# Kernel optimization log

Measured on AMD Instinct MI355X. Metric: run time of the kernel, lower is better.

Reference implementation:

```python
import jax, jax.numpy as jnp
import numpy as np

B, T, EMB, NDIM = 8, 2048, 1024, 1024


def setup_inputs() -> dict:
    key = jax.random.key(0)
    k1, k2, k3, k4 = jax.random.split(key, 4)
    X = jax.random.normal(k1, (B, T, EMB), dtype=jnp.float32)
    # Linear(emb, ndim, bias=False); stored as [emb, ndim] so projection is X @ W.
    scale = 1.0 / np.sqrt(EMB)
    Wq = jax.random.normal(k2, (EMB, NDIM), dtype=jnp.float32) * scale
    Wk = jax.random.normal(k3, (EMB, NDIM), dtype=jnp.float32) * scale
    Wv = jax.random.normal(k4, (EMB, NDIM), dtype=jnp.float32) * scale
    return {"X": X, "Wq": Wq, "Wk": Wk, "Wv": Wv}


def reference(X, Wq, Wk, Wv):
    ndim = Wq.shape[-1]
    T_ = X.shape[1]
    Q = X @ Wq  # [B,T,ndim]
    K = X @ Wk  # [B,T,ndim]
    V = X @ Wv  # [B,T,ndim]
    # scores[b,t,s] = Q[b,t] . K[b,s], scaled by ndim^-0.5
    scores = jnp.einsum("btd,bsd->bts", Q, K) * (ndim ** -0.5)
    mask = jnp.tril(jnp.ones((T_, T_), dtype=bool))  # causal lower-triangular
    scores = jnp.where(mask, scores, -jnp.inf)
    # NOTE: source uses F.softmax(..., dim=1) -> normalize over the QUERY axis
    # (columns of the [T,T] matrix), not the usual key axis. Replicated faithfully.
    probs = jax.nn.softmax(scores, axis=1)
    # dropout is identity in eval / p=0 deterministic baseline
    return probs @ V  # [B,T,ndim]
```

## Files before the change

kernel.cpp:

```cpp
#include <hip/hip_runtime.h>
#include <hip/hip_bf16.h>

#define B_   8
#define T_   2048
#define EMB_ 1024
#define ND_  1024
#define NTB2 8

typedef __attribute__((ext_vector_type(8))) short   bf8_t;
typedef __attribute__((ext_vector_type(4))) float   f32x4;

__device__ __forceinline__ unsigned short f2bf(float f) {
  union { float f; unsigned int u; } c; c.f = f;
  unsigned int u = c.u;
  unsigned int r = (u + 0x7FFFu + ((u >> 16) & 1u)) >> 16;
  return (unsigned short)r;
}

__device__ __forceinline__ float bf2f(unsigned short b) {
  union { unsigned int u; float f; } c; c.u = ((unsigned int)b) << 16;
  return c.f;
}

__device__ __forceinline__ void gload_lds16(const unsigned short* g, unsigned short* l) {
  __builtin_amdgcn_global_load_lds(
      (const __attribute__((address_space(1))) unsigned int*)g,
      (__attribute__((address_space(3))) unsigned int*)l,
      16, 0, 0);
}

#define SB0() __builtin_amdgcn_sched_barrier(0)
#define BAR() __builtin_amdgcn_s_barrier()

__device__ __forceinline__ void stage_half(const unsigned short* __restrict__ g, int lda,
                                           unsigned short* lhalf, int wave, int lane) {
  const int r3 = lane >> 3, c3 = lane & 7;
  const int colsw = ((c3 ^ r3) << 3);
#pragma unroll
  for (int j = 0; j < 2; ++j) {
    const int row = wave * 8 + r3 + 64 * j;
    gload_lds16(g + (size_t)row * lda + colsw, lhalf + wave * 512 + j * 4096);
  }
}

__device__ __forceinline__ bf8_t read_frag(const unsigned short* half, int r, int ks, int lane) {
  const int col = (((ks) << 5) + ((lane >> 4) << 3)) ^ ((r & 7) << 3);
  return *(const bf8_t*)(half + r * 64 + col);
}

__device__ __forceinline__ int swz_ep(int x) { return ((x >> 1) & 7) << 4; }

__global__ void __launch_bounds__(256) cvt_x_kernel(const float* __restrict__ in,
                                                    unsigned short* __restrict__ out) {
  const int i = (blockIdx.x * 256 + threadIdx.x) * 4;
  float4 v = *(const float4*)(in + i);
  ushort4 o = make_ushort4(f2bf(v.x), f2bf(v.y), f2bf(v.z), f2bf(v.w));
  *(ushort4*)(out + i) = o;
}

__global__ void __launch_bounds__(256) transpose_w3_kernel(const float* __restrict__ Wq,
                                                           const float* __restrict__ Wk,
                                                           const float* __restrict__ Wv,
                                                           unsigned short* __restrict__ Wt3) {
  __shared__ unsigned short tile[32][33];
  const int z = blockIdx.z;
  const float* W = (z == 0) ? Wq : (z == 1) ? Wk : Wv;
  const float cscale = (z == 0) ? 0.03125f : 1.0f;
  unsigned short* Wt = Wt3 + (size_t)z * ND_ * EMB_;
  const int n0 = blockIdx.x * 32, k0 = blockIdx.y * 32;
  const int tx = threadIdx.x & 31, ty = threadIdx.x >> 5;
#pragma unroll
  for (int r = 0; r < 32; r += 8) {
    float v = W[(size_t)(k0 + ty + r) * ND_ + n0 + tx];
    tile[tx][ty + r] = f2bf(v * cscale);
  }
  __syncthreads();
#pragma unroll
  for (int r = 0; r < 32; r += 8) {
    Wt[(size_t)(n0 + ty + r) * EMB_ + k0 + tx] = tile[ty + r][tx];
  }
}

#define MFMA_QUAD(MB, AF, AOFF) do { \
  __builtin_amdgcn_s_setprio(1); \
  _Pragma("unroll") \
  for (int mi = 0; mi < 2; ++mi) \
    _Pragma("unroll") \
    for (int nf = 0; nf < 4; ++nf) \
      _Pragma("unroll") \
      for (int ks = 0; ks < 2; ++ks) \
        acc[(MB) * 2 + mi][nf] = __builtin_amdgcn_mfma_f32_16x16x32_bf16( \
            (AF)[(AOFF) + mi][ks], bfr[nf][ks], acc[(MB) * 2 + mi][nf], 0, 0, 0); \
  __builtin_amdgcn_s_setprio(0); \
} while (0)

#define MFMA_Q8(MB) do { \
  __builtin_amdgcn_s_setprio(1); \
  _Pragma("unroll") \
  for (int nf = 0; nf < 4; ++nf) \
    _Pragma("unroll") \
    for (int ks = 0; ks < 2; ++ks) \
      acc[(MB)][nf] = __builtin_amdgcn_mfma_f32_16x16x32_bf16( \
          af[(MB)][ks], bfr[nf][ks], acc[(MB)][nf], 0, 0, 0); \
  __builtin_amdgcn_s_setprio(0); \
} while (0)

#define LDSA(d, h) (lds256 + ((d) * 2 + (h)) * 8192)
#define LDSB(d, h) (lds256 + 32768 + ((d) * 2 + (h)) * 8192)

#define GEMM256_LOOP(ABASE, BBASE, LDK) \
  stage_half((ABASE),                             (LDK), LDSA(0, 0), wave, lane); \
  stage_half((ABASE) + (size_t)128 * (LDK),       (LDK), LDSA(0, 1), wave, lane); \
  stage_half((BBASE),                             (LDK), LDSB(0, 0), wave, lane); \
  stage_half((BBASE) + (size_t)128 * (LDK),       (LDK), LDSB(0, 1), wave, lane); \
  stage_half((BBASE) + 64,                        (LDK), LDSB(1, 0), wave, lane); \
  stage_half((BBASE) + (size_t)128 * (LDK) + 64,  (LDK), LDSB(1, 1), wave, lane); \
  stage_half((ABASE) + 64,                        (LDK), LDSA(1, 0), wave, lane); \
  stage_half((ABASE) + (size_t)128 * (LDK) + 64,  (LDK), LDSA(1, 1), wave, lane); \
  asm volatile("s_waitcnt vmcnt(8)" ::: "memory"); \
  SB0(); BAR(); SB0(); \
  for (int t = 0; t < 16; ++t) { \
    const int d = t & 1; \
    const unsigned short* Ah = LDSA(d, wm); \
    const unsigned short* Bh = LDSB(d, wn >> 1); \
    bf8_t bfr[4][2], af[4][2]; \
    _Pragma("unroll") \
    for (int nf = 0; nf < 4; ++nf) \
      _Pragma("unroll") \
      for (int ks = 0; ks < 2; ++ks) bfr[nf][ks] = read_frag(Bh, brow + nf * 16, ks, lane); \
    _Pragma("unroll") \
    for (int mf = 0; mf < 4; ++mf) \
      _Pragma("unroll") \
      for (int ks = 0; ks < 2; ++ks) af[mf][ks] = read_frag(Ah, arow + mf * 16, ks, lane); \
    SB0(); BAR(); SB0(); \
    MFMA_QUAD(0, af, 0); \
    SB0(); \
    asm volatile("s_waitcnt lgkmcnt(0)" ::: "memory"); \
    SB0(); BAR(); SB0(); \
    if (t < 14) { \
      stage_half((BBASE) + (size_t)(t + 2) * 64,                     (LDK), LDSB(d, 0), wave, lane); \
      stage_half((BBASE) + (size_t)128 * (LDK) + (size_t)(t + 2) * 64,(LDK), LDSB(d, 1), wave, lane); \
    } \
    SB0(); BAR(); SB0(); \
    MFMA_QUAD(1, af, 2); \
    SB0(); BAR(); SB0(); \
    bf8_t af2[4][2]; \
    _Pragma("unroll") \
    for (int mf = 0; mf < 4; ++mf) \
      _Pragma("unroll") \
      for (int ks = 0; ks < 2; ++ks) af2[mf][ks] = read_frag(Ah, arow + (mf + 4) * 16, ks, lane); \
    SB0(); BAR(); SB0(); \
    MFMA_QUAD(2, af2, 0); \
    SB0(); \
    asm volatile("s_waitcnt lgkmcnt(0)" ::: "memory"); \
    SB0(); BAR(); SB0(); \
    if (t < 14) { \
      stage_half((ABASE) + (size_t)(t + 2) * 64,                     (LDK), LDSA(d, 0), wave, lane); \
      stage_half((ABASE) + (size_t)128 * (LDK) + (size_t)(t + 2) * 64,(LDK), LDSA(d, 1), wave, lane); \
      asm volatile("s_waitcnt vmcnt(8)" ::: "memory"); \
    } else if (t == 14) { \
      asm volatile("s_waitcnt vmcnt(0)" ::: "memory"); \
    } \
    SB0(); BAR(); SB0(); \
    MFMA_QUAD(3, af2, 2); \
    SB0(); BAR(); SB0(); \
  }

template <int OUTMODE>
__global__ void __launch_bounds__(512, 2)
gemm_xw256_kernel(const unsigned short* __restrict__ A,
                  const unsigned short* __restrict__ Bt,
                  unsigned short* __restrict__ C) {
  extern __shared__ unsigned short lds256[];
  const int tid = threadIdx.x, lane = tid & 63, wave = tid >> 6;
  const int wm = wave >> 2, wn = wave & 3;
  const int m0 = blockIdx.y * 256, n0 = blockIdx.x * 256;
  const unsigned short* Ab = A + (size_t)m0 * EMB_;
  const unsigned short* Bb = Bt + (size_t)n0 * EMB_;
  f32x4 acc[8][4];
#pragma unroll
  for (int i = 0; i < 8; ++i)
#pragma unroll
    for (int j = 0; j < 4; ++j)
#pragma unroll
      for (int q = 0; q < 4; ++q) acc[i][j][q] = 0.f;
  const int arow = lane & 15;
  const int brow = (wn & 1) * 64 + (lane & 15);

  GEMM256_LOOP(Ab, Bb, EMB_)

  const int cc = lane & 15, cr4 = (lane >> 4) << 2;
#pragma unroll
  for (int mf = 0; mf < 8; ++mf)
#pragma unroll
    for (int nf = 0; nf < 4; ++nf)
#pragma unroll
      for (int q = 0; q < 4; ++q) {
        const int r = wm * 128 + mf * 16 + cr4 + q;
        const int c = wn * 64 + nf * 16 + cc;
        const unsigned short bv = f2bf(acc[mf][nf][q]);
        const int byte = (OUTMODE == 1) ? (c * 512 + ((r * 2) ^ swz_ep(c)))
                                        : (r * 512 + ((c * 2) ^ swz_ep(r)));
        lds256[byte >> 1] = bv;
      }
  __syncthreads();
  if (OUTMODE == 0) {
#pragma unroll
    for (int p = 0; p < 16; ++p) {
      const int o = p * 8192 + tid * 16;
      const int ri = o >> 9, cb = o & 511;
      const bf8_t v = *(const bf8_t*)(lds256 + (((o & ~511) | (cb ^ swz_ep(ri))) >> 1));
      *(bf8_t*)(C + (size_t)(m0 + ri) * ND_ + n0 + (cb >> 1)) = v;
    }
  } else {
    const int bb = m0 >> 11, tt0 = m0 & 2047;
#pragma unroll
    for (int p = 0; p < 16; ++p) {
      const int o = p * 8192 + tid * 16;
      const int ci = o >> 9, rb = o & 511;
      const bf8_t v = *(const bf8_t*)(lds256 + (((o & ~511) | (rb ^ swz_ep(ci))) >> 1));
      *(bf8_t*)(C + ((size_t)bb * ND_ + n0 + ci) * T_ + tt0 + (rb >> 1)) = v;
    }
  }
}

__global__ void __launch_bounds__(512, 2)
scoretile576_kernel(const unsigned short* __restrict__ Qb,
                    const unsigned short* __restrict__ Kb,
                    unsigned short* __restrict__ Pp,
                    float* __restrict__ pm) {
  extern __shared__ unsigned short lds256[];
  const int id = blockIdx.x;
  const int b = id & 7;
  const int r = id >> 3;
  int sc = 0, pfx = 0;
#pragma unroll 8
  for (int i = 0; i < 8; ++i) {
    const int cnt = 16 - 2 * sc;
    if (pfx + cnt <= r) { pfx += cnt; ++sc; }
  }
  const int tr = 2 * sc + (r - pfx);
  const int t0 = tr * 128, s0 = sc * 256;
  const int tid = threadIdx.x, lane = tid & 63, wave = tid >> 6;
  const int wm = wave >> 2, wn = wave & 3;
  const int arow = lane & 15;
  const unsigned short* Ab = Qb + ((size_t)b * T_ + t0) * ND_;
  const unsigned short* Bb = Kb + ((size_t)b * T_ + s0) * ND_;
  f32x4 acc[4][4];
#pragma unroll
  for (int i = 0; i < 4; ++i)
#pragma unroll
    for (int j = 0; j < 4; ++j)
#pragma unroll
      for (int q = 0; q < 4; ++q) acc[i][j][q] = 0.f;

  stage_half(Ab,                           ND_, lds256,                     wave, lane);
  stage_half(Bb,                           ND_, lds256 + 16384,             wave, lane);
  stage_half(Bb + (size_t)128 * ND_,       ND_, lds256 + 16384 + 8192,      wave, lane);
  stage_half(Ab + 64,                      ND_, lds256 + 8192,              wave, lane);
  stage_half(Bb + 64,                      ND_, lds256 + 16384 + 2 * 8192,  wave, lane);
  stage_half(Bb + (size_t)128 * ND_ + 64,  ND_, lds256 + 16384 + 3 * 8192,  wave, lane);
  asm volatile("s_waitcnt vmcnt(6)" ::: "memory");
  SB0(); BAR(); SB0();

  for (int t = 0; t < 16; ++t) {
    const int d = t & 1;
    const unsigned short* Ah = lds256 + d * 8192;
    const unsigned short* Bh = lds256 + 16384 + (d * 2 + (wn >> 1)) * 8192;
    bf8_t bfr[4][2], af[4][2];
#pragma unroll
    for (int nf = 0; nf < 4; ++nf)
#pragma unroll
      for (int ks = 0; ks < 2; ++ks)
        bfr[nf][ks] = read_frag(Bh, (wn & 1) * 64 + nf * 16 + arow, ks, lane);
#pragma unroll
    for (int mf = 0; mf < 4; ++mf)
#pragma unroll
      for (int ks = 0; ks < 2; ++ks)
        af[mf][ks] = read_frag(Ah, wm * 64 + mf * 16 + arow, ks, lane);
    SB0(); BAR(); SB0();
    MFMA_Q8(0);
    SB0();
    asm volatile("s_waitcnt lgkmcnt(0)" ::: "memory");
    SB0(); BAR(); SB0();
    if (t < 14) {
      stage_half(Ab + (size_t)(t + 2) * 64, ND_, lds256 + d * 8192, wave, lane);
      stage_half(Bb + (size_t)(t + 2) * 64, ND_, lds256 + 16384 + (d * 2) * 8192, wave, lane);
    }
    SB0(); BAR(); SB0();
    MFMA_Q8(1);
    SB0(); BAR(); SB0();
    if (t < 14)
      stage_half(Bb + (size_t)128 * ND_ + (size_t)(t + 2) * 64, ND_, lds256 + 16384 + (d * 2 + 1) * 8192, wave, lane);
    SB0(); BAR(); SB0();
    MFMA_Q8(2);
    SB0(); BAR(); SB0();
    if (t < 14)      { asm volatile("s_waitcnt vmcnt(6)" ::: "memory"); }
    else if (t == 14){ asm volatile("s_waitcnt vmcnt(0)" ::: "memory"); }
    SB0(); BAR(); SB0();
    MFMA_Q8(3);
    SB0(); BAR(); SB0();
  }

  __syncthreads();
  const int cc = lane & 15, cr4 = (lane >> 4) << 2;
  float csum[4];
#pragma unroll
  for (int nf = 0; nf < 4; ++nf) csum[nf] = 0.f;
#pragma unroll
  for (int mf = 0; mf < 4; ++mf)
#pragma unroll
    for (int nf = 0; nf < 4; ++nf)
#pragma unroll
      for (int q = 0; q < 4; ++q) {
        const int rr = wm * 64 + mf * 16 + cr4 + q;
        const int c  = wn * 64 + nf * 16 + cc;
        const bool ok = (t0 + rr) >= (s0 + c);
        unsigned short bv = 0;
        if (ok) {
          bv = f2bf(__expf(fminf(acc[mf][nf][q], 30.f)));
          csum[nf] += bf2f(bv);
        }
        lds256[(rr * 512 + ((c * 2) ^ swz_ep(rr))) >> 1] = bv;
      }
  __syncthreads();
  unsigned short* Pbase = Pp + (size_t)b * T_ * T_;
#pragma unroll
  for (int p = 0; p < 8; ++p) {
    const int o = p * 8192 + tid * 16;
    const int ri = o >> 9, cb = o & 511;
    const bf8_t v = *(const bf8_t*)(lds256 + (((o & ~511) | (cb ^ swz_ep(ri))) >> 1));
    *(bf8_t*)(Pbase + (size_t)(t0 + ri) * T_ + s0 + (cb >> 1)) = v;
  }
#pragma unroll
  for (int nf = 0; nf < 4; ++nf) {
    csum[nf] += __shfl_xor(csum[nf], 16);
    csum[nf] += __shfl_xor(csum[nf], 32);
  }
  __syncthreads();
  float* red = (float*)lds256;
  if (lane < 16) {
#pragma unroll
    for (int nf = 0; nf < 4; ++nf)
      red[((wm * 4 + wn) * 4 + nf) * 16 + lane] = csum[nf];
  }
  __syncthreads();
  if (wm == 0 && lane < 16) {
    const size_t base = (((size_t)b * 8 + sc) * 16 + tr) * 256;
#pragma unroll
    for (int nf = 0; nf < 4; ++nf) {
      const float s = red[((0 * 4 + wn) * 4 + nf) * 16 + lane] +
                      red[((1 * 4 + wn) * 4 + nf) * 16 + lane];
      pm[base + wn * 64 + nf * 16 + lane] = s;
    }
  }
}

__global__ void __launch_bounds__(256) colreduce_kernel(const float* __restrict__ pm,
                                                        float* __restrict__ colinv) {
  const int sc = blockIdx.x, b = blockIdx.y, c = threadIdx.x;
  float l = 0.f;
  for (int tr = 2 * sc; tr < 16; ++tr)
    l += pm[(((size_t)b * 8 + sc) * 16 + tr) * 256 + c];
  colinv[(size_t)b * T_ + sc * 256 + c] = 1.0f / l;
}

__global__ void __launch_bounds__(256) vscale_kernel(unsigned short* __restrict__ Vt,
                                                     const float* __restrict__ colinv) {
  const int idx = blockIdx.x * 256 + threadIdx.x;
  const int s8 = (idx * 8) & (T_ - 1);
  const int bd = idx / (T_ / 8);
  const int b = bd >> 10;
  unsigned short* p = Vt + (size_t)bd * T_ + s8;
  bf8_t v = *(bf8_t*)p;
#pragma unroll
  for (int j = 0; j < 8; ++j) {
    const float f = bf2f((unsigned short)v[j]) * colinv[(size_t)b * T_ + s8 + j];
    v[j] = (short)f2bf(f);
  }
  *(bf8_t*)p = v;
}

__device__ __forceinline__ void pv_segment(const unsigned short* __restrict__ Ab,
                                           const unsigned short* __restrict__ Bb,
                                           float* __restrict__ Cb,
                                           int ktiles, unsigned short* lds256,
                                           int lane, int wave) {
  const int wm = wave >> 2, wn = wave & 3;
  const int arow = lane & 15;
  f32x4 acc[4][4];
#pragma unroll
  for (int i = 0; i < 4; ++i)
#pragma unroll
    for (int j = 0; j < 4; ++j)
#pragma unroll
      for (int q = 0; q < 4; ++q) acc[i][j][q] = 0.f;

  stage_half(Ab,                           T_, lds256,                     wave, lane);
  stage_half(Bb,                           T_, lds256 + 16384,             wave, lane);
  stage_half(Bb + (size_t)128 * T_,        T_, lds256 + 16384 + 8192,      wave, lane);
  stage_half(Ab + 64,                      T_, lds256 + 8192,              wave, lane);
  stage_half(Bb + 64,                      T_, lds256 + 16384 + 2 * 8192,  wave, lane);
  stage_half(Bb + (size_t)128 * T_ + 64,   T_, lds256 + 16384 + 3 * 8192,  wave, lane);
  asm volatile("s_waitcnt vmcnt(6)" ::: "memory");
  SB0(); BAR(); SB0();

  for (int t = 0; t < ktiles; ++t) {
    const int d = t & 1;
    const unsigned short* Ah = lds256 + d * 8192;
    const unsigned short* Bh = lds256 + 16384 + (d * 2 + (wn >> 1)) * 8192;
    bf8_t bfr[4][2], af[4][2];
#pragma unroll
    for (int nf = 0; nf < 4; ++nf)
#pragma unroll
      for (int ks = 0; ks < 2; ++ks)
        bfr[nf][ks] = read_frag(Bh, (wn & 1) * 64 + nf * 16 + arow, ks, lane);
#pragma unroll
    for (int mf = 0; mf < 4; ++mf)
#pragma unroll
      for (int ks = 0; ks < 2; ++ks)
        af[mf][ks] = read_frag(Ah, wm * 64 + mf * 16 + arow, ks, lane);
    SB0(); BAR(); SB0();
    MFMA_Q8(0);
    SB0();
    asm volatile("s_waitcnt lgkmcnt(0)" ::: "memory");
    SB0(); BAR(); SB0();
    if (t < ktiles - 2) {
      stage_half(Ab + (size_t)(t + 2) * 64, T_, lds256 + d * 8192, wave, lane);
      stage_half(Bb + (size_t)(t + 2) * 64, T_, lds256 + 16384 + (d * 2) * 8192, wave, lane);
    }
    SB0(); BAR(); SB0();
    MFMA_Q8(1);
    SB0(); BAR(); SB0();
    if (t < ktiles - 2)
      stage_half(Bb + (size_t)128 * T_ + (size_t)(t + 2) * 64, T_, lds256 + 16384 + (d * 2 + 1) * 8192, wave, lane);
    SB0(); BAR(); SB0();
    MFMA_Q8(2);
    SB0(); BAR(); SB0();
    if (t < ktiles - 2)      { asm volatile("s_waitcnt vmcnt(6)" ::: "memory"); }
    else if (t == ktiles - 2){ asm volatile("s_waitcnt vmcnt(0)" ::: "memory"); }
    SB0(); BAR(); SB0();
    MFMA_Q8(3);
    SB0(); BAR(); SB0();
  }

  const int cc = lane & 15, cr4 = (lane >> 4) << 2;
#pragma unroll
  for (int mf = 0; mf < 4; ++mf)
#pragma unroll
    for (int nf = 0; nf < 4; ++nf)
#pragma unroll
      for (int q = 0; q < 4; ++q) {
        const int row = wm * 64 + mf * 16 + cr4 + q;
        const int col = wn * 64 + nf * 16 + cc;
        Cb[(size_t)row * ND_ + col] = acc[mf][nf][q];
      }
}

__global__ void __launch_bounds__(512, 2)
gemm_pv256_kernel(const unsigned short* __restrict__ Pb,
                  const unsigned short* __restrict__ Vt,
                  float* __restrict__ out) {
  extern __shared__ unsigned short lds256[];
  const int b = blockIdx.x & 7;
  const int pair = (blockIdx.x >> 3) & 7;
  const int ncol = blockIdx.x >> 6;
  const int lane = threadIdx.x & 63, wave = threadIdx.x >> 6;
  const int tbs[2] = {pair, 15 - pair};
#pragma unroll
  for (int si = 0; si < 2; ++si) {
    const int tb = tbs[si];
    const int ktiles = 2 * tb + 2;
    pv_segment(Pb + (size_t)b * T_ * T_ + (size_t)tb * 128 * T_,
               Vt + (size_t)b * ND_ * T_ + (size_t)ncol * 256 * T_,
               out + (size_t)b * T_ * ND_ + (size_t)tb * 128 * ND_ + ncol * 256,
               ktiles, lds256, lane, wave);
  }
}

extern "C" void kernel_launch(void* const* d_in, const int* in_sizes, int n_in,
                              void* d_out, int out_size, void* d_ws, size_t ws_size,
                              hipStream_t stream) {
  const float* X  = (const float*)d_in[0];
  const float* Wq = (const float*)d_in[1];
  const float* Wk = (const float*)d_in[2];
  const float* Wv = (const float*)d_in[3];
  float* out = (float*)d_out;
  (void)in_sizes; (void)n_in; (void)out_size;

  char* ws = (char*)d_ws;
  size_t off = 0;
  auto alloc = [&](size_t bytes) {
    void* p = ws + off;
    off += (bytes + 255) & ~(size_t)255;
    return p;
  };
  unsigned short* Xb  = (unsigned short*)alloc((size_t)B_ * T_ * EMB_ * 2);
  unsigned short* Wt3 = (unsigned short*)alloc((size_t)3 * ND_ * EMB_ * 2);
  unsigned short* Qb  = (unsigned short*)alloc((size_t)B_ * T_ * ND_ * 2);
  unsigned short* Kb  = (unsigned short*)alloc((size_t)B_ * T_ * ND_ * 2);
  unsigned short* Vt  = (unsigned short*)alloc((size_t)B_ * ND_ * T_ * 2);
  float* colinv = (float*)alloc((size_t)B_ * T_ * 4);
  float* pm     = (float*)alloc((size_t)B_ * 8 * 16 * 256 * 4);
  unsigned short* Pb  = (unsigned short*)alloc((size_t)B_ * T_ * T_ * 2);
  if (off > ws_size) return;

  hipFuncSetAttribute((const void*)&gemm_xw256_kernel<0>,
                      hipFuncAttributeMaxDynamicSharedMemorySize, 131072);
  hipFuncSetAttribute((const void*)&gemm_xw256_kernel<1>,
                      hipFuncAttributeMaxDynamicSharedMemorySize, 131072);
  hipFuncSetAttribute((const void*)&scoretile576_kernel,
                      hipFuncAttributeMaxDynamicSharedMemorySize, 98304);
  hipFuncSetAttribute((const void*)&gemm_pv256_kernel,
                      hipFuncAttributeMaxDynamicSharedMemorySize, 98304);

  hipLaunchKernelGGL(cvt_x_kernel, dim3((B_ * T_ * EMB_) / 1024), dim3(256), 0, stream, X, Xb);
  hipLaunchKernelGGL(transpose_w3_kernel, dim3(32, 32, 3), dim3(256), 0, stream, Wq, Wk, Wv, Wt3);
  hipLaunchKernelGGL((gemm_xw256_kernel<0>), dim3(ND_ / 256, (B_ * T_) / 256), dim3(512), 131072, stream,
                     Xb, Wt3, Qb);
  hipLaunchKernelGGL((gemm_xw256_kernel<0>), dim3(ND_ / 256, (B_ * T_) / 256), dim3(512), 131072, stream,
                     Xb, Wt3 + (size_t)ND_ * EMB_, Kb);
  hipLaunchKernelGGL((gemm_xw256_kernel<1>), dim3(ND_ / 256, (B_ * T_) / 256), dim3(512), 131072, stream,
                     Xb, Wt3 + (size_t)2 * ND_ * EMB_, Vt);
  hipLaunchKernelGGL(scoretile576_kernel, dim3(576), dim3(512), 98304, stream, Qb, Kb, Pb, pm);
  hipLaunchKernelGGL(colreduce_kernel, dim3(8, B_), dim3(256), 0, stream, pm, colinv);
  hipLaunchKernelGGL(vscale_kernel, dim3((B_ * ND_ * T_) / 8 / 256), dim3(256), 0, stream, Vt, colinv);
  hipLaunchKernelGGL(gemm_pv256_kernel, dim3(NTB2 * 4 * B_), dim3(512), 98304, stream, Pb, Vt, out);
}
```

Baseline: 283.0 us.

## Retile causal score kernel to 128x128 triangular tiles with higher occupancy

The score/exp kernel moves from 128x256 tiles (576 blocks) to 128x128 tiles enumerated over the lower triangle with a sqrt-based decode (1088 blocks). Causal masking is applied only on diagonal tiles, and LDS use drops to 64KB so launch bounds allow 4 blocks per CU. The aim is to cut wasted upper-triangle work and improve load balance and occupancy. In exchange, each smaller tile reuses less of what it loads, and the column-sum partials and colreduce are re-laid out for 128-wide column blocks. Blocks just above the diagonal are no longer written as zeros, so correctness depends on the PV GEMM never reading them.

```diff
diff --git a/kernel.cpp b/kernel.cpp
--- a/kernel.cpp
+++ b/kernel.cpp
@@ -29,6 +29,14 @@
       16, 0, 0);
 }
 
+__device__ __forceinline__ void tri_decode(int p, int& tblk, int& sblk) {
+  int t = (int)((sqrtf(8.0f * (float)p + 1.0f) - 1.0f) * 0.5f);
+  while ((t + 1) * (t + 2) / 2 <= p) ++t;
+  while (t * (t + 1) / 2 > p) --t;
+  tblk = t;
+  sblk = p - t * (t + 1) / 2;
+}
+
 #define SB0() __builtin_amdgcn_sched_barrier(0)
 #define BAR() __builtin_amdgcn_s_barrier()
 
@@ -49,6 +57,7 @@
 }
 
 __device__ __forceinline__ int swz_ep(int x) { return ((x >> 1) & 7) << 4; }
+__device__ __forceinline__ int swz_ep2(int r) { return (r & 7) << 4; }
 
 __global__ void __launch_bounds__(256) cvt_x_kernel(const float* __restrict__ in,
                                                     unsigned short* __restrict__ out) {
@@ -98,6 +107,17 @@
   __builtin_amdgcn_s_setprio(1); \
   _Pragma("unroll") \
   for (int nf = 0; nf < 4; ++nf) \
+    _Pragma("unroll") \
+    for (int ks = 0; ks < 2; ++ks) \
+      acc[(MB)][nf] = __builtin_amdgcn_mfma_f32_16x16x32_bf16( \
+          af[(MB)][ks], bfr[nf][ks], acc[(MB)][nf], 0, 0, 0); \
+  __builtin_amdgcn_s_setprio(0); \
+} while (0)
+
+#define MFMA_Q4(MB) do { \
+  __builtin_amdgcn_s_setprio(1); \
+  _Pragma("unroll") \
+  for (int nf = 0; nf < 2; ++nf) \
     _Pragma("unroll") \
     for (int ks = 0; ks < 2; ++ks) \
       acc[(MB)][nf] = __builtin_amdgcn_mfma_f32_16x16x32_bf16( \
@@ -224,116 +244,105 @@
   }
 }
 
-__global__ void __launch_bounds__(512, 2)
-scoretile576_kernel(const unsigned short* __restrict__ Qb,
-                    const unsigned short* __restrict__ Kb,
-                    unsigned short* __restrict__ Pp,
-                    float* __restrict__ pm) {
+__global__ void __launch_bounds__(512, 4)
+scoretile1088_kernel(const unsigned short* __restrict__ Qb,
+                     const unsigned short* __restrict__ Kb,
+                     unsigned short* __restrict__ Pp,
+                     float* __restrict__ pm) {
   extern __shared__ unsigned short lds256[];
   const int id = blockIdx.x;
   const int b = id & 7;
-  const int r = id >> 3;
-  int sc = 0, pfx = 0;
-#pragma unroll 8
-  for (int i = 0; i < 8; ++i) {
-    const int cnt = 16 - 2 * sc;
-    if (pfx + cnt <= r) { pfx += cnt; ++sc; }
-  }
-  const int tr = 2 * sc + (r - pfx);
-  const int t0 = tr * 128, s0 = sc * 256;
+  int tb, sb;
+  tri_decode(id >> 3, tb, sb);
+  const int t0 = tb * 128, s0 = sb * 128;
   const int tid = threadIdx.x, lane = tid & 63, wave = tid >> 6;
   const int wm = wave >> 2, wn = wave & 3;
   const int arow = lane & 15;
   const unsigned short* Ab = Qb + ((size_t)b * T_ + t0) * ND_;
   const unsigned short* Bb = Kb + ((size_t)b * T_ + s0) * ND_;
-  f32x4 acc[4][4];
+  f32x4 acc[4][2];
 #pragma unroll
   for (int i = 0; i < 4; ++i)
 #pragma unroll
-    for (int j = 0; j < 4; ++j)
+    for (int j = 0; j < 2; ++j)
 #pragma unroll
       for (int q = 0; q < 4; ++q) acc[i][j][q] = 0.f;
 
-  stage_half(Ab,                           ND_, lds256,                     wave, lane);
-  stage_half(Bb,                           ND_, lds256 + 16384,             wave, lane);
-  stage_half(Bb + (size_t)128 * ND_,       ND_, lds256 + 16384 + 8192,      wave, lane);
-  stage_half(Ab + 64,                      ND_, lds256 + 8192,              wave, lane);
-  stage_half(Bb + 64,                      ND_, lds256 + 16384 + 2 * 8192,  wave, lane);
-  stage_half(Bb + (size_t)128 * ND_ + 64,  ND_, lds256 + 16384 + 3 * 8192,  wave, lane);
-  asm volatile("s_waitcnt vmcnt(6)" ::: "memory");
+  stage_half(Ab,      ND_, lds256,                 wave, lane);
+  stage_half(Bb,      ND_, lds256 + 16384,         wave, lane);
+  stage_half(Ab + 64, ND_, lds256 + 8192,          wave, lane);
+  stage_half(Bb + 64, ND_, lds256 + 16384 + 8192,  wave, lane);
+  asm volatile("s_waitcnt vmcnt(4)" ::: "memory");
   SB0(); BAR(); SB0();
 
   for (int t = 0; t < 16; ++t) {
     const int d = t & 1;
     const unsigned short* Ah = lds256 + d * 8192;
-    const unsigned short* Bh = lds256 + 16384 + (d * 2 + (wn >> 1)) * 8192;
-    bf8_t bfr[4][2], af[4][2];
-#pragma unroll
-    for (int nf = 0; nf < 4; ++nf)
+    const unsigned short* Bh = lds256 + 16384 + d * 8192;
+    bf8_t bfr[2][2], af[4][2];
+#pragma unroll
+    for (int nf = 0; nf < 2; ++nf)
 #pragma unroll
       for (int ks = 0; ks < 2; ++ks)
-        bfr[nf][ks] = read_frag(Bh, (wn & 1) * 64 + nf * 16 + arow, ks, lane);
+        bfr[nf][ks] = read_frag(Bh, wn * 32 + nf * 16 + arow, ks, lane);
 #pragma unroll
     for (int mf = 0; mf < 4; ++mf)
 #pragma unroll
       for (int ks = 0; ks < 2; ++ks)
         af[mf][ks] = read_frag(Ah, wm * 64 + mf * 16 + arow, ks, lane);
     SB0(); BAR(); SB0();
-    MFMA_Q8(0);
+    MFMA_Q4(0);
     SB0();
     asm volatile("s_waitcnt lgkmcnt(0)" ::: "memory");
     SB0(); BAR(); SB0();
-    if (t < 14) {
-      stage_half(Ab + (size_t)(t + 2) * 64, ND_, lds256 + d * 8192, wave, lane);
-      stage_half(Bb + (size_t)(t + 2) * 64, ND_, lds256 + 16384 + (d * 2) * 8192, wave, lane);
-    }
-    SB0(); BAR(); SB0();
-    MFMA_Q8(1);
-    SB0(); BAR(); SB0();
-    if (t < 14)
-      stage_half(Bb + (size_t)128 * ND_ + (size_t)(t + 2) * 64, ND_, lds256 + 16384 + (d * 2 + 1) * 8192, wave, lane);
-    SB0(); BAR(); SB0();
-    MFMA_Q8(2);
-    SB0(); BAR(); SB0();
-    if (t < 14)      { asm volatile("s_waitcnt vmcnt(6)" ::: "memory"); }
+    if (t < 14) stage_half(Ab + (size_t)(t + 2) * 64, ND_, lds256 + d * 8192, wave, lane);
+    SB0(); BAR(); SB0();
+    MFMA_Q4(1);
+    SB0(); BAR(); SB0();
+    if (t < 14) stage_half(Bb + (size_t)(t + 2) * 64, ND_, lds256 + 16384 + d * 8192, wave, lane);
+    SB0(); BAR(); SB0();
+    MFMA_Q4(2);
+    SB0(); BAR(); SB0();
+    if (t < 14)      { asm volatile("s_waitcnt vmcnt(4)" ::: "memory"); }
     else if (t == 14){ asm volatile("s_waitcnt vmcnt(0)" ::: "memory"); }
     SB0(); BAR(); SB0();
-    MFMA_Q8(3);
+    MFMA_Q4(3);
     SB0(); BAR(); SB0();
   }
 
   __syncthreads();
   const int cc = lane & 15, cr4 = (lane >> 4) << 2;
-  float csum[4];
-#pragma unroll
-  for (int nf = 0; nf < 4; ++nf) csum[nf] = 0.f;
+  const bool diag = (tb == sb);
+  float csum[2];
+#pragma unroll
+  for (int nf = 0; nf < 2; ++nf) csum[nf] = 0.f;
 #pragma unroll
   for (int mf = 0; mf < 4; ++mf)
 #pragma unroll
-    for (int nf = 0; nf < 4; ++nf)
+    for (int nf = 0; nf < 2; ++nf)
 #pragma unroll
       for (int q = 0; q < 4; ++q) {
         const int rr = wm * 64 + mf * 16 + cr4 + q;
-        const int c  = wn * 64 + nf * 16 + cc;
-        const bool ok = (t0 + rr) >= (s0 + c);
+        const int c  = wn * 32 + nf * 16 + cc;
+        const bool ok = !diag || ((t0 + rr) >= (s0 + c));
         unsigned short bv = 0;
         if (ok) {
           bv = f2bf(__expf(fminf(acc[mf][nf][q], 30.f)));
           csum[nf] += bf2f(bv);
         }
-        lds256[(rr * 512 + ((c * 2) ^ swz_ep(rr))) >> 1] = bv;
+        lds256[(rr * 256 + ((c * 2) ^ swz_ep2(rr))) >> 1] = bv;
       }
   __syncthreads();
   unsigned short* Pbase = Pp + (size_t)b * T_ * T_;
 #pragma unroll
-  for (int p = 0; p < 8; ++p) {
+  for (int p = 0; p < 4; ++p) {
     const int o = p * 8192 + tid * 16;
-    const int ri = o >> 9, cb = o & 511;
-    const bf8_t v = *(const bf8_t*)(lds256 + (((o & ~511) | (cb ^ swz_ep(ri))) >> 1));
+    const int ri = o >> 8, cb = o & 255;
+    const bf8_t v = *(const bf8_t*)(lds256 + (((o & ~255) | (cb ^ swz_ep2(ri))) >> 1));
     *(bf8_t*)(Pbase + (size_t)(t0 + ri) * T_ + s0 + (cb >> 1)) = v;
   }
 #pragma unroll
-  for (int nf = 0; nf < 4; ++nf) {
+  for (int nf = 0; nf < 2; ++nf) {
     csum[nf] += __shfl_xor(csum[nf], 16);
     csum[nf] += __shfl_xor(csum[nf], 32);
   }
@@ -341,28 +350,28 @@
   float* red = (float*)lds256;
   if (lane < 16) {
 #pragma unroll
-    for (int nf = 0; nf < 4; ++nf)
-      red[((wm * 4 + wn) * 4 + nf) * 16 + lane] = csum[nf];
+    for (int nf = 0; nf < 2; ++nf)
+      red[((wm * 4 + wn) * 2 + nf) * 16 + lane] = csum[nf];
   }
   __syncthreads();
   if (wm == 0 && lane < 16) {
-    const size_t base = (((size_t)b * 8 + sc) * 16 + tr) * 256;
-#pragma unroll
-    for (int nf = 0; nf < 4; ++nf) {
-      const float s = red[((0 * 4 + wn) * 4 + nf) * 16 + lane] +
-                      red[((1 * 4 + wn) * 4 + nf) * 16 + lane];
-      pm[base + wn * 64 + nf * 16 + lane] = s;
+    const size_t base = (((size_t)b * 16 + sb) * 16 + tb) * 128;
+#pragma unroll
+    for (int nf = 0; nf < 2; ++nf) {
+      const float s = red[((0 * 4 + wn) * 2 + nf) * 16 + lane] +
+                      red[((1 * 4 + wn) * 2 + nf) * 16 + lane];
+      pm[base + wn * 32 + nf * 16 + lane] = s;
     }
   }
 }
 
-__global__ void __launch_bounds__(256) colreduce_kernel(const float* __restrict__ pm,
+__global__ void __launch_bounds__(128) colreduce_kernel(const float* __restrict__ pm,
                                                         float* __restrict__ colinv) {
-  const int sc = blockIdx.x, b = blockIdx.y, c = threadIdx.x;
+  const int sb = blockIdx.x, b = blockIdx.y, c = threadIdx.x;
   float l = 0.f;
-  for (int tr = 2 * sc; tr < 16; ++tr)
-    l += pm[(((size_t)b * 8 + sc) * 16 + tr) * 256 + c];
-  colinv[(size_t)b * T_ + sc * 256 + c] = 1.0f / l;
+  for (int tb = sb; tb < 16; ++tb)
+    l += pm[(((size_t)b * 16 + sb) * 16 + tb) * 128 + c];
+  colinv[(size_t)b * T_ + sb * 128 + c] = 1.0f / l;
 }
 
 __global__ void __launch_bounds__(256) vscale_kernel(unsigned short* __restrict__ Vt,
@@ -501,7 +510,7 @@
   unsigned short* Kb  = (unsigned short*)alloc((size_t)B_ * T_ * ND_ * 2);
   unsigned short* Vt  = (unsigned short*)alloc((size_t)B_ * ND_ * T_ * 2);
   float* colinv = (float*)alloc((size_t)B_ * T_ * 4);
-  float* pm     = (float*)alloc((size_t)B_ * 8 * 16 * 256 * 4);
+  float* pm     = (float*)alloc((size_t)B_ * 16 * 16 * 128 * 4);
   unsigned short* Pb  = (unsigned short*)alloc((size_t)B_ * T_ * T_ * 2);
   if (off > ws_size) return;
 
@@ -509,8 +518,8 @@
                       hipFuncAttributeMaxDynamicSharedMemorySize, 131072);
   hipFuncSetAttribute((const void*)&gemm_xw256_kernel<1>,
                       hipFuncAttributeMaxDynamicSharedMemorySize, 131072);
-  hipFuncSetAttribute((const void*)&scoretile576_kernel,
-                      hipFuncAttributeMaxDynamicSharedMemorySize, 98304);
+  hipFuncSetAttribute((const void*)&scoretile1088_kernel,
+                      hipFuncAttributeMaxDynamicSharedMemorySize, 65536);
   hipFuncSetAttribute((const void*)&gemm_pv256_kernel,
                       hipFuncAttributeMaxDynamicSharedMemorySize, 98304);
 
@@ -522,8 +531,8 @@
                      Xb, Wt3 + (size_t)ND_ * EMB_, Kb);
   hipLaunchKernelGGL((gemm_xw256_kernel<1>), dim3(ND_ / 256, (B_ * T_) / 256), dim3(512), 131072, stream,
                      Xb, Wt3 + (size_t)2 * ND_ * EMB_, Vt);
-  hipLaunchKernelGGL(scoretile576_kernel, dim3(576), dim3(512), 98304, stream, Qb, Kb, Pb, pm);
-  hipLaunchKernelGGL(colreduce_kernel, dim3(8, B_), dim3(256), 0, stream, pm, colinv);
+  hipLaunchKernelGGL(scoretile1088_kernel, dim3(136 * B_), dim3(512), 65536, stream, Qb, Kb, Pb, pm);
+  hipLaunchKernelGGL(colreduce_kernel, dim3(16, B_), dim3(128), 0, stream, pm, colinv);
   hipLaunchKernelGGL(vscale_kernel, dim3((B_ * ND_ * T_) / 8 / 256), dim3(256), 0, stream, Vt, colinv);
   hipLaunchKernelGGL(gemm_pv256_kernel, dim3(NTB2 * 4 * B_), dim3(512), 98304, stream, Pb, Vt, out);
 }
```

Result: faster. 267.0 us (-5.7%).
